# Kernel tuning notes

Measured on AMD Instinct MI355X. Metric: run time of the kernel, lower is better.

The kernel has to match this reference:

```python
import jax, jax.numpy as jnp
import numpy as np
from jax import lax

S, T, B = 32, 32, 512          # src len, tgt len, batch
H, E, A = 1024, 256, 1024      # hidden, embed, attention dim
VS, VT = 64, 70                # source / target char vocab
START = 1                      # data.tar_l2i[start_token]


def _gru_cell(gi, h, W_hh, b_hh):
    """torch GRUCell math. gi = x @ W_ih.T + b_ih, shape (B, 3H)."""
    gh = h @ W_hh.T + b_hh
    ir, iz, in_ = jnp.split(gi, 3, axis=-1)
    hr, hz, hn = jnp.split(gh, 3, axis=-1)
    r = jax.nn.sigmoid(ir + hr)
    z = jax.nn.sigmoid(iz + hz)
    n = jnp.tanh(in_ + r * hn)
    return (1.0 - z) * n + z * h


def setup_inputs() -> dict:
    key = jax.random.key(0)
    ks = jax.random.split(key, 16)
    n = lambda k, shp: jax.random.normal(k, shp, dtype=jnp.float32) * 0.05
    return {
        "source": jax.random.randint(ks[0], (S, B), 0, VS),
        "target": jax.random.randint(ks[1], (T, B), 0, VT),
        "teacher_forcing": 1,
        "emb_src": n(ks[2], (VS, E)),
        "W_ih_enc": n(ks[3], (3 * H, E)),
        "W_hh_enc": n(ks[4], (3 * H, H)),
        "b_ih_enc": n(ks[5], (3 * H,)),
        "b_hh_enc": n(ks[6], (3 * H,)),
        "emb_tgt": n(ks[7], (VT, E)),
        "W_attn": n(ks[8], (2 * H, A)),
        "b_attn": n(ks[9], (A,)),
        "v_attn": n(ks[10], (A,)),
        "W_ih_dec": n(ks[11], (3 * H, H + E)),
        "W_hh_dec": n(ks[12], (3 * H, H)),
        "b_ih_dec": n(ks[13], (3 * H,)),
        "b_hh_dec": n(ks[14], (3 * H,)),
        "W_out": n(ks[15], (H, VT)),
        "b_out": jnp.zeros((VT,), jnp.float32),
    }


def reference(source, target, teacher_forcing, emb_src, W_ih_enc, W_hh_enc,
              b_ih_enc, b_hh_enc, emb_tgt, W_attn, b_attn, v_attn,
              W_ih_dec, W_hh_dec, b_ih_dec, b_hh_dec, W_out, b_out):
    tf = bool(teacher_forcing)

    # ---------------- Encoder: GRU over (S, B) ----------------
    x_emb = emb_src[source]                                   # (S, B, E)
    # precompute input-to-hidden GEMM for all timesteps (big fused GEMM)
    gi_all = jnp.einsum('sbe,ge->sbg', x_emb, W_ih_enc) + b_ih_enc  # (S, B, 3H)

    def enc_step(h, gi_t):
        h = _gru_cell(gi_t, h, W_hh_enc, b_hh_enc)
        return h, h

    h0 = jnp.zeros((B, H), x_emb.dtype)
    h_enc, enc_ops = lax.scan(enc_step, h0, gi_all)           # enc_ops: (S, B, H)

    # ---------------- Decoder loop (t = 1 .. T-1) ----------------
    def dec_step(carry, tgt_t):
        h, x = carry
        emb = emb_tgt[x]                                      # (B, E)
        hx = jnp.broadcast_to(h[None], (S, B, H))
        feat = jnp.concatenate([hx, enc_ops], axis=-1)        # (S, B, 2H)
        energy = jnp.tanh(jnp.einsum('sbf,fa->sba', feat, W_attn) + b_attn)
        scores = energy @ v_attn                              # (S, B)
        alpha = jax.nn.softmax(scores, axis=0)                # over source positions
        ctx = jnp.einsum('sb,sbh->bh', alpha, enc_ops)        # (B, H)
        gi = jnp.concatenate([ctx, emb], axis=-1) @ W_ih_dec.T + b_ih_dec
        h_new = _gru_cell(gi, h, W_hh_dec, b_hh_dec)
        logits = h_new @ W_out + b_out                        # (B, VT)
        x_next = tgt_t if tf else jnp.argmax(logits, axis=1)
        return (h_new, x_next), (logits, alpha.T)             # attn row: (B, S)

    (_, _), (dec_logits, attn) = lax.scan(dec_step, (h_enc, target[0]), target[1:])

    # outputs[0] is the one-hot start token (outputs[:, :, start]=1, rows 1.. overwritten)
    row0 = jnp.zeros((B, VT), dec_logits.dtype).at[:, START].set(1.0)
    outputs = jnp.concatenate([row0[None], dec_logits], axis=0)  # (T, B, VT)
    return outputs, attn                                         # attn: (T-1, B, S)
```

## Files before the change

### kernel.cpp

```cpp
#include <hip/hip_runtime.h>
#include <hip/hip_bf16.h>

typedef __bf16 bfx8 __attribute__((ext_vector_type(8)));
typedef __bf16 bfx4 __attribute__((ext_vector_type(4)));
typedef float f32x4 __attribute__((ext_vector_type(4)));

#define MFMA __builtin_amdgcn_mfma_f32_16x16x32_bf16


__device__ __attribute__((aligned(256))) float  g_h[512 * 1024];
__device__ __attribute__((aligned(256))) float  g_hpart[512 * 1024];
__device__ __attribute__((aligned(256))) __bf16 g_hb[2][512 * 1024];
__device__ __attribute__((aligned(256))) __bf16 g_Adec[512 * 1280];
__device__ __attribute__((aligned(256))) __bf16 g_enc_ops[(size_t)32 * 512 * 1024];
__device__ __attribute__((aligned(256))) __bf16 g_enc_part[(size_t)32 * 512 * 1024];
__device__ __attribute__((aligned(256))) __bf16 g_sWhhe[(size_t)3072 * 1024];
__device__ __attribute__((aligned(256))) __bf16 g_sWihe[(size_t)3072 * 256];
__device__ __attribute__((aligned(256))) __bf16 g_sWhhd[(size_t)3072 * 1024];
__device__ __attribute__((aligned(256))) __bf16 g_sWihd[(size_t)3072 * 1280];
__device__ __attribute__((aligned(256))) __bf16 g_sWattnA[(size_t)1024 * 1024];
__device__ __attribute__((aligned(256))) __bf16 g_sWattnB[(size_t)1024 * 1024];
__device__ __attribute__((aligned(256))) __bf16 g_sWout[(size_t)128 * 1024];
__device__ __attribute__((aligned(256))) __bf16 g_embs[64 * 256];
__device__ __attribute__((aligned(256))) __bf16 g_embt[70 * 256];

__device__ __forceinline__ float fast_tanh(float x) {
    float cx = fminf(fmaxf(x, -15.f), 15.f);
    float e = __expf(-2.f * cx);
    return (1.f - e) / (1.f + e);
}

__global__ void k_cvt(const float* __restrict__ src, __bf16* __restrict__ dst,
                      int n4)
{
    int i = blockIdx.x * 256 + threadIdx.x;
    if (i >= n4) return;
    float4 v = ((const float4*)src)[i];
    __bf16 o[4] = {(__bf16)v.x, (__bf16)v.y, (__bf16)v.z, (__bf16)v.w};
    *(ushort2*)(dst + 4 * i) = *(ushort2*)o;
    *(ushort2*)(dst + 4 * i + 2) = *(ushort2*)(o + 2);
}

__global__ void swz_rm(const float* __restrict__ W, __bf16* __restrict__ out,
                       int nK, int total)
{
    int gid = blockIdx.x * 256 + threadIdx.x;
    if (gid >= total) return;
    int F = gid >> 6, L = gid & 63;
    int t = F / nK, c = F - t * nK;
    int K = nK * 32;
    const float* s = W + (size_t)(t * 16 + (L & 15)) * K + c * 32 + (L >> 4) * 8;
    __bf16 o[8];
#pragma unroll
    for (int u = 0; u < 8; u++) o[u] = (__bf16)s[u];
    *(uint4*)(out + (size_t)gid * 8) = *(uint4*)o;
}

__global__ void swz_cm(const float* __restrict__ W, __bf16* __restrict__ out,
                       int nK, int ldsrc, int nguard, int total)
{
    int gid = blockIdx.x * 256 + threadIdx.x;
    if (gid >= total) return;
    int F = gid >> 6, L = gid & 63;
    int t = F / nK, c = F - t * nK;
    int n = t * 16 + (L & 15);
    int k = c * 32 + (L >> 4) * 8;
    __bf16 o[8];
#pragma unroll
    for (int u = 0; u < 8; u++)
        o[u] = (n < nguard) ? (__bf16)W[(size_t)(k + u) * ldsrc + n] : (__bf16)0.f;
    *(uint4*)(out + (size_t)gid * 8) = *(uint4*)o;
}

__global__ void k_init(float* __restrict__ out)
{
    int idx = blockIdx.x * 256 + threadIdx.x;
    if (idx < 512 * 1024) { g_h[idx] = 0.f; g_hb[0][idx] = (__bf16)0.f; }
    if (idx < 512 * 70) out[idx] = (idx % 70 == 1) ? 1.f : 0.f;
}

__global__ __launch_bounds__(512, 1) void k_encpart(
    const __bf16* __restrict__ Amat, const __bf16* __restrict__ sW,
    __bf16* __restrict__ Cout)
{
    __shared__ __bf16 sA[64 * 1024];
    const int tid = threadIdx.x;
    const int w = tid >> 6, lane = tid & 63;
    const int r15 = lane & 15, q = lane >> 4;
    const int n0 = blockIdx.x * 256, m0 = blockIdx.y * 64;

#pragma unroll
    for (int i = 0; i < 16; i++) {
        int lin = tid + i * 512;
        int r = lin >> 7, U = lin & 127;
        uint4 v = *(const uint4*)(Amat + (size_t)(m0 + r) * 1024 + U * 8);
        *(uint4*)(sA + (r * 128 + (U ^ (r & 7))) * 8) = v;
    }
    __syncthreads();

    const int xk = r15 & 7;
    f32x4 acc[2][4];
#pragma unroll
    for (int nn = 0; nn < 2; nn++)
#pragma unroll
        for (int mf = 0; mf < 4; mf++) acc[nn][mf] = (f32x4){0.f, 0.f, 0.f, 0.f};

    const __bf16* wp0 = sW + ((size_t)(blockIdx.x * 16 + w * 2) * 32) * 512 + lane * 8;
    const __bf16* wp1 = wp0 + 32 * 512;
    const int ar0 = r15 * 1024;
    const int ar1 = (16 + r15) * 1024;
    const int ar2 = (32 + r15) * 1024;
    const int ar3 = (48 + r15) * 1024;

#pragma unroll 4
    for (int c = 0; c < 32; c++) {
        int us = ((c * 4 + q) ^ xk) * 8;
        bfx8 a0 = *(const bfx8*)(sA + ar0 + us);
        bfx8 a1 = *(const bfx8*)(sA + ar1 + us);
        bfx8 a2 = *(const bfx8*)(sA + ar2 + us);
        bfx8 a3 = *(const bfx8*)(sA + ar3 + us);
        bfx8 w0 = *(const bfx8*)(wp0 + c * 512);
        bfx8 w1 = *(const bfx8*)(wp1 + c * 512);
        acc[0][0] = MFMA(a0, w0, acc[0][0], 0, 0, 0);
        acc[0][1] = MFMA(a1, w0, acc[0][1], 0, 0, 0);
        acc[0][2] = MFMA(a2, w0, acc[0][2], 0, 0, 0);
        acc[0][3] = MFMA(a3, w0, acc[0][3], 0, 0, 0);
        acc[1][0] = MFMA(a0, w1, acc[1][0], 0, 0, 0);
        acc[1][1] = MFMA(a1, w1, acc[1][1], 0, 0, 0);
        acc[1][2] = MFMA(a2, w1, acc[1][2], 0, 0, 0);
        acc[1][3] = MFMA(a3, w1, acc[1][3], 0, 0, 0);
    }

#pragma unroll
    for (int nn = 0; nn < 2; nn++) {
        const int col = n0 + (w * 2 + nn) * 16 + r15;
#pragma unroll
        for (int mf = 0; mf < 4; mf++) {
#pragma unroll
            for (int reg = 0; reg < 4; reg++) {
                int row = m0 + mf * 16 + q * 4 + reg;
                Cout[(size_t)row * 1024 + col] = (__bf16)acc[nn][mf][reg];
            }
        }
    }
}

__global__ __launch_bounds__(512, 1) void gru_step(
    const __bf16* __restrict__ hb_in, __bf16* __restrict__ hb_out,
    const __bf16* __restrict__ sW1, const float* __restrict__ b1,
    const __bf16* __restrict__ sW2, const float* __restrict__ b2,
    int nK2, const int* __restrict__ src_t, int enc_t)
{
    __shared__ __bf16 sA1[32 * 1024];
    __shared__ __bf16 sA2[32 * 1280];
    const int tid = threadIdx.x;
    const int w = tid >> 6, lane = tid & 63;
    const int r15 = lane & 15, q = lane >> 4;
    const int j0 = blockIdx.x * 64, m0 = blockIdx.y * 32;
    const int jsub = w & 3;

#pragma unroll
    for (int i = 0; i < 8; i++) {
        int lin = tid + i * 512;
        int r = lin >> 7, U = lin & 127;
        uint4 v = *(const uint4*)(hb_in + (size_t)(m0 + r) * 1024 + U * 8);
        *(uint4*)(sA1 + (r * 128 + (U ^ (r & 7))) * 8) = v;
    }
    if (src_t) {
#pragma unroll
        for (int i = 0; i < 2; i++) {
            int lin = tid + i * 512;
            int r = lin >> 5, U = lin & 31;
            int sv = src_t[m0 + r];
            sv = (sv < 0) ? 0 : (sv > 63 ? 63 : sv);
            uint4 v = *(const uint4*)(g_embs + sv * 256 + U * 8);
            *(uint4*)(sA2 + (r * 32 + (U ^ (r & 7))) * 8) = v;
        }
    } else {
        for (int lin = tid; lin < 32 * 160; lin += 512) {
            int r = lin / 160, U = lin - r * 160;
            uint4 v = *(const uint4*)(g_Adec + (size_t)(m0 + r) * 1280 + U * 8);
            *(uint4*)(sA2 + (r * 160 + (U ^ (r & 7))) * 8) = v;
        }
    }
    __syncthreads();

    const size_t tb = (size_t)(blockIdx.x * 4 + jsub);
    const int xk = r15 & 7;
    f32x4 acc[3][2];
#pragma unroll
    for (int s = 0; s < 3; s++)
#pragma unroll
        for (int ms = 0; ms < 2; ms++) acc[s][ms] = (f32x4){0.f, 0.f, 0.f, 0.f};

    if (w < 4) {
        const __bf16* wp0 = sW1 + (tb * 32) * 512 + lane * 8;
        const __bf16* wp1 = sW1 + ((tb + 64) * 32) * 512 + lane * 8;
        const __bf16* wp2 = sW1 + ((tb + 128) * 32) * 512 + lane * 8;
        const int ar0 = r15 * 1024, ar1 = (16 + r15) * 1024;
#pragma unroll 4
        for (int c = 0; c < 32; c++) {
            int us = ((c * 4 + q) ^ xk) * 8;
            bfx8 a0 = *(const bfx8*)(sA1 + ar0 + us);
            bfx8 a1 = *(const bfx8*)(sA1 + ar1 + us);
            bfx8 w0 = *(const bfx8*)(wp0 + c * 512);
            bfx8 w1 = *(const bfx8*)(wp1 + c * 512);
            bfx8 w2 = *(const bfx8*)(wp2 + c * 512);
            acc[0][0] = MFMA(a0, w0, acc[0][0], 0, 0, 0);
            acc[0][1] = MFMA(a1, w0, acc[0][1], 0, 0, 0);
            acc[1][0] = MFMA(a0, w1, acc[1][0], 0, 0, 0);
            acc[1][1] = MFMA(a1, w1, acc[1][1], 0, 0, 0);
            acc[2][0] = MFMA(a0, w2, acc[2][0], 0, 0, 0);
            acc[2][1] = MFMA(a1, w2, acc[2][1], 0, 0, 0);
        }
    } else {
        const __bf16* wp0 = sW2 + (tb * (size_t)nK2) * 512 + lane * 8;
        const __bf16* wp1 = sW2 + ((tb + 64) * (size_t)nK2) * 512 + lane * 8;
        const __bf16* wp2 = sW2 + ((tb + 128) * (size_t)nK2) * 512 + lane * 8;
        const int ru = nK2 * 4;
        const int ar0 = r15 * ru * 8, ar1 = (16 + r15) * ru * 8;
#pragma unroll 4
        for (int c = 0; c < nK2; c++) {
            int us = ((c * 4 + q) ^ xk) * 8;
            bfx8 a0 = *(const bfx8*)(sA2 + ar0 + us);
            bfx8 a1 = *(const bfx8*)(sA2 + ar1 + us);
            bfx8 w0 = *(const bfx8*)(wp0 + c * 512);
            bfx8 w1 = *(const bfx8*)(wp1 + c * 512);
            bfx8 w2 = *(const bfx8*)(wp2 + c * 512);
            acc[0][0] = MFMA(a0, w0, acc[0][0], 0, 0, 0);
            acc[0][1] = MFMA(a1, w0, acc[0][1], 0, 0, 0);
            acc[1][0] = MFMA(a0, w1, acc[1][0], 0, 0, 0);
            acc[1][1] = MFMA(a1, w1, acc[1][1], 0, 0, 0);
            acc[2][0] = MFMA(a0, w2, acc[2][0], 0, 0, 0);
            acc[2][1] = MFMA(a1, w2, acc[2][1], 0, 0, 0);
        }
    }
    __syncthreads();
    float* sGi = (float*)sA2;
    if (w >= 4) {
#pragma unroll
        for (int s = 0; s < 3; s++)
#pragma unroll
            for (int ms = 0; ms < 2; ms++)
#pragma unroll
                for (int reg = 0; reg < 4; reg++)
                    sGi[((s * 4 + jsub) * 32 + ms * 16 + q * 4 + reg) * 16 + r15] =
                        acc[s][ms][reg];
    }
    __syncthreads();
    if (w < 4) {
        const int jj = j0 + jsub * 16 + r15;
        const float bb1[3] = {b1[jj], b1[1024 + jj], b1[2048 + jj]};
        const float bb2[3] = {b2[jj], b2[1024 + jj], b2[2048 + jj]};
#pragma unroll
        for (int ms = 0; ms < 2; ms++) {
#pragma unroll
            for (int reg = 0; reg < 4; reg++) {
                int bl = ms * 16 + q * 4 + reg;
                int b_ = m0 + bl;
                float gh0 = acc[0][ms][reg] + bb1[0];
                float gh1 = acc[1][ms][reg] + bb1[1];
                float gh2 = acc[2][ms][reg] + bb1[2];
                float gi0 = sGi[((0 * 4 + jsub) * 32 + bl) * 16 + r15] + bb2[0];
                float gi1 = sGi[((1 * 4 + jsub) * 32 + bl) * 16 + r15] + bb2[1];
                float gi2 = sGi[((2 * 4 + jsub) * 32 + bl) * 16 + r15] + bb2[2];
                float r = 1.f / (1.f + __expf(-(gi0 + gh0)));
                float z = 1.f / (1.f + __expf(-(gi1 + gh1)));
                float n = fast_tanh(gi2 + r * gh2);
                size_t off = (size_t)b_ * 1024 + jj;
                float hv = (1.f - z) * n + z * g_h[off];
                g_h[off] = hv;
                hb_out[off] = (__bf16)hv;
                if (enc_t >= 0)
                    g_enc_ops[(size_t)enc_t * 524288 + off] = (__bf16)hv;
            }
        }
    }
}

__global__ __launch_bounds__(256) void k_hl(
    const __bf16* __restrict__ src, const float* __restrict__ battn,
    const float* __restrict__ bout, int lrow, float* __restrict__ outp)
{
    __shared__ __bf16 sA[32 * 1024];
    const int tid = threadIdx.x;
    const int w = tid >> 6, lane = tid & 63;
    const int r15 = lane & 15, q = lane >> 4;
    const int bx = blockIdx.x, m0 = blockIdx.y * 32;

#pragma unroll
    for (int i = 0; i < 16; i++) {
        int lin = tid + i * 256;
        int r = lin >> 7, U = lin & 127;
        uint4 v = *(const uint4*)(src + (size_t)(m0 + r) * 1024 + U * 8);
        *(uint4*)(sA + (r * 128 + (U ^ (r & 7))) * 8) = v;
    }
    __syncthreads();

    const __bf16* sW;
    int n;
    if (bx < 16) {
        sW = g_sWattnA;
        n = bx * 64 + w * 16 + r15;
    } else {
        if (lrow < 0) return;
        sW = g_sWout;
        n = (bx - 16) * 64 + w * 16 + r15;
    }
    const size_t tb = (size_t)((bx < 16 ? bx : bx - 16) * 4 + w);
    const __bf16* wp = sW + (tb * 32) * 512 + lane * 8;
    const int xk = r15 & 7;
    const int ar0 = r15 * 1024, ar1 = (16 + r15) * 1024;

    f32x4 acc[2];
    acc[0] = (f32x4){0.f, 0.f, 0.f, 0.f};
    acc[1] = (f32x4){0.f, 0.f, 0.f, 0.f};
#pragma unroll 4
    for (int c = 0; c < 32; c++) {
        int us = ((c * 4 + q) ^ xk) * 8;
        bfx8 a0 = *(const bfx8*)(sA + ar0 + us);
        bfx8 a1 = *(const bfx8*)(sA + ar1 + us);
        bfx8 wv = *(const bfx8*)(wp + c * 512);
        acc[0] = MFMA(a0, wv, acc[0], 0, 0, 0);
        acc[1] = MFMA(a1, wv, acc[1], 0, 0, 0);
    }

    if (bx < 16) {
        float bv = battn[n];
#pragma unroll
        for (int ms = 0; ms < 2; ms++)
#pragma unroll
            for (int reg = 0; reg < 4; reg++)
                g_hpart[(size_t)(m0 + ms * 16 + q * 4 + reg) * 1024 + n] =
                    acc[ms][reg] + bv;
    } else if (n < 70) {
        float bv = bout[n];
#pragma unroll
        for (int ms = 0; ms < 2; ms++)
#pragma unroll
            for (int reg = 0; reg < 4; reg++)
                outp[(size_t)lrow * 35840 +
                     (size_t)(m0 + ms * 16 + q * 4 + reg) * 70 + n] =
                    acc[ms][reg] + bv;
    }
}

__global__ __launch_bounds__(256) void k_attn(
    int j, const int* __restrict__ target, const int* __restrict__ tf,
    const float* __restrict__ v_attn, float* __restrict__ out)
{
    const int b = blockIdx.x, tid = threadIdx.x;
    const int lane = tid & 63, wave = tid >> 6;
    __shared__ float sc[32], sal[32];
    __shared__ int sx;
    if (wave == 0) {
        int xv;
        if (j == 0) xv = target[b];
        else if (*tf) xv = target[j * 512 + b];
        else {
            const float* row = out + (size_t)j * 35840 + b * 70;
            float bv = row[lane]; int bi = lane;
            if (lane < 6) {
                float v2 = row[lane + 64];
                if (v2 > bv) { bv = v2; bi = lane + 64; }
            }
#pragma unroll
            for (int off = 32; off; off >>= 1) {
                float ov = __shfl_down(bv, off);
                int   oi = __shfl_down(bi, off);
                if (ov > bv || (ov == bv && oi < bi)) { bv = ov; bi = oi; }
            }
            xv = bi;
        }
        if (lane == 0) sx = (xv < 0) ? 0 : (xv > 69 ? 69 : xv);
    }
    float hpv[16], vsv[16];
    {
        const float* hp = g_hpart + (size_t)b * 1024;
#pragma unroll
        for (int u = 0; u < 8; u++) {
            hpv[u]     = hp[lane * 8 + u];
            hpv[8 + u] = hp[512 + lane * 8 + u];
            vsv[u]     = v_attn[lane * 8 + u];
            vsv[8 + u] = v_attn[512 + lane * 8 + u];
        }
    }
    __syncthreads();
    g_Adec[(size_t)b * 1280 + 1024 + tid] = g_embt[sx * 256 + tid];
    for (int s = wave * 8; s < wave * 8 + 8; s++) {
        const __bf16* ep = g_enc_part + ((size_t)s * 512 + b) * 1024;
        bfx8 e0 = *(const bfx8*)(ep + lane * 8);
        bfx8 e1 = *(const bfx8*)(ep + 512 + lane * 8);
        float part = 0.f;
#pragma unroll
        for (int u = 0; u < 8; u++) {
            part += vsv[u]     * fast_tanh((float)e0[u] + hpv[u]);
            part += vsv[8 + u] * fast_tanh((float)e1[u] + hpv[8 + u]);
        }
#pragma unroll
        for (int off = 32; off; off >>= 1) part += __shfl_down(part, off);
        if (lane == 0) sc[s] = part;
    }
    __syncthreads();
    float mx = sc[0];
#pragma unroll
    for (int s = 1; s < 32; s++) mx = fmaxf(mx, sc[s]);
    float den = 0.f;
#pragma unroll
    for (int s = 0; s < 32; s++) den += __expf(sc[s] - mx);
    float rden = 1.f / den;
    if (tid < 32) {
        float al = __expf(sc[tid] - mx) * rden;
        sal[tid] = al;
        out[1146880 + (size_t)j * 16384 + b * 32 + tid] = al;
    }
    __syncthreads();
    float c0 = 0, c1 = 0, c2 = 0, c3 = 0;
    const __bf16* eo = g_enc_ops + (size_t)b * 1024 + tid * 4;
#pragma unroll 4
    for (int s = 0; s < 32; s++) {
        bfx4 e = *(const bfx4*)(eo + (size_t)s * 524288);
        float al = sal[s];
        c0 += al * (float)e[0]; c1 += al * (float)e[1];
        c2 += al * (float)e[2]; c3 += al * (float)e[3];
    }
    bfx4 o = {(__bf16)c0, (__bf16)c1, (__bf16)c2, (__bf16)c3};
    *(bfx4*)(&g_Adec[(size_t)b * 1280 + tid * 4]) = o;
}

extern "C" void kernel_launch(void* const* d_in, const int* in_sizes, int n_in,
                              void* d_out, int out_size, void* d_ws, size_t ws_size,
                              hipStream_t stream)
{
    const int*   source   = (const int*)d_in[0];
    const int*   target   = (const int*)d_in[1];
    const int*   tf       = (const int*)d_in[2];
    const float* emb_src  = (const float*)d_in[3];
    const float* W_ih_enc = (const float*)d_in[4];
    const float* W_hh_enc = (const float*)d_in[5];
    const float* b_ih_enc = (const float*)d_in[6];
    const float* b_hh_enc = (const float*)d_in[7];
    const float* emb_tgt  = (const float*)d_in[8];
    const float* W_attn   = (const float*)d_in[9];
    const float* b_attn   = (const float*)d_in[10];
    const float* v_attn   = (const float*)d_in[11];
    const float* W_ih_dec = (const float*)d_in[12];
    const float* W_hh_dec = (const float*)d_in[13];
    const float* b_ih_dec = (const float*)d_in[14];
    const float* b_hh_dec = (const float*)d_in[15];
    const float* W_out    = (const float*)d_in[16];
    const float* b_out    = (const float*)d_in[17];
    float* out = (float*)d_out;

    void *p_hb, *p_sWhhe, *p_sWihe, *p_sWhhd, *p_sWihd, *p_sWattnA, *p_sWattnB,
         *p_sWout, *p_embs, *p_embt, *p_enc_ops, *p_enc_part;
    hipGetSymbolAddress(&p_hb,       HIP_SYMBOL(g_hb));
    hipGetSymbolAddress(&p_sWhhe,    HIP_SYMBOL(g_sWhhe));
    hipGetSymbolAddress(&p_sWihe,    HIP_SYMBOL(g_sWihe));
    hipGetSymbolAddress(&p_sWhhd,    HIP_SYMBOL(g_sWhhd));
    hipGetSymbolAddress(&p_sWihd,    HIP_SYMBOL(g_sWihd));
    hipGetSymbolAddress(&p_sWattnA,  HIP_SYMBOL(g_sWattnA));
    hipGetSymbolAddress(&p_sWattnB,  HIP_SYMBOL(g_sWattnB));
    hipGetSymbolAddress(&p_sWout,    HIP_SYMBOL(g_sWout));
    hipGetSymbolAddress(&p_embs,     HIP_SYMBOL(g_embs));
    hipGetSymbolAddress(&p_embt,     HIP_SYMBOL(g_embt));
    hipGetSymbolAddress(&p_enc_ops,  HIP_SYMBOL(g_enc_ops));
    hipGetSymbolAddress(&p_enc_part, HIP_SYMBOL(g_enc_part));
    __bf16* hb0 = (__bf16*)p_hb;
    __bf16* hb1 = hb0 + 512 * 1024;

    k_cvt<<<16, 256, 0, stream>>>(emb_src, (__bf16*)p_embs, 64 * 256 / 4);
    k_cvt<<<18, 256, 0, stream>>>(emb_tgt, (__bf16*)p_embt, 70 * 256 / 4);
    swz_rm<<<1536, 256, 0, stream>>>(W_hh_enc, (__bf16*)p_sWhhe, 32, 393216);
    swz_rm<<<384,  256, 0, stream>>>(W_ih_enc, (__bf16*)p_sWihe, 8,  98304);
    swz_rm<<<1536, 256, 0, stream>>>(W_hh_dec, (__bf16*)p_sWhhd, 32, 393216);
    swz_rm<<<1920, 256, 0, stream>>>(W_ih_dec, (__bf16*)p_sWihd, 40, 491520);
    swz_cm<<<512,  256, 0, stream>>>(W_attn, (__bf16*)p_sWattnA, 32, 1024, 1024, 131072);
    swz_cm<<<512,  256, 0, stream>>>(W_attn + (size_t)1024 * 1024,
                                     (__bf16*)p_sWattnB, 32, 1024, 1024, 131072);
    swz_cm<<<64,   256, 0, stream>>>(W_out,  (__bf16*)p_sWout,   32, 70,   70,   16384);
    k_init<<<2048, 256, 0, stream>>>(out);

    for (int t = 0; t < 32; t++) {
        __bf16* hin  = (t & 1) ? hb1 : hb0;
        __bf16* hout = (t & 1) ? hb0 : hb1;
        gru_step<<<dim3(16, 16), 512, 0, stream>>>(
            hin, hout, (__bf16*)p_sWhhe, b_hh_enc,
            (__bf16*)p_sWihe, b_ih_enc, 8, source + t * 512, t);
    }

    k_encpart<<<dim3(4, 256), 512, 0, stream>>>(
        (__bf16*)p_enc_ops, (__bf16*)p_sWattnB, (__bf16*)p_enc_part);

    k_hl<<<dim3(18, 16), 256, 0, stream>>>(hb0, b_attn, b_out, -1, out);

    for (int j = 0; j < 31; j++) {
        __bf16* hin  = (j & 1) ? hb1 : hb0;
        __bf16* hout = (j & 1) ? hb0 : hb1;
        k_attn<<<512, 256, 0, stream>>>(j, target, tf, v_attn, out);
        gru_step<<<dim3(16, 16), 512, 0, stream>>>(
            hin, hout, (__bf16*)p_sWhhd, b_hh_dec,
            (__bf16*)p_sWihd, b_ih_dec, 40, nullptr, -1);
        k_hl<<<dim3(18, 16), 256, 0, stream>>>(hout, b_attn, b_out, j + 1, out);
    }
}
```

Measured before the change: 2.551 ms.

## Double-buffer encoder input GEMM and rebalance GRU step K-loop across warps

Result: no change. 2.550 ms (-0.1%).

```diff
diff --git a/kernel.cpp b/kernel.cpp
--- a/kernel.cpp
+++ b/kernel.cpp
@@ -79,23 +79,32 @@
     if (idx < 512 * 70) out[idx] = (idx % 70 == 1) ? 1.f : 0.f;
 }
 
-__global__ __launch_bounds__(512, 1) void k_encpart(
+__global__ __launch_bounds__(512, 4) void k_encpart(
     const __bf16* __restrict__ Amat, const __bf16* __restrict__ sW,
     __bf16* __restrict__ Cout)
 {
-    __shared__ __bf16 sA[64 * 1024];
+    __shared__ __bf16 sA[2][64 * 256];
     const int tid = threadIdx.x;
     const int w = tid >> 6, lane = tid & 63;
     const int r15 = lane & 15, q = lane >> 4;
     const int n0 = blockIdx.x * 256, m0 = blockIdx.y * 64;
 
-#pragma unroll
-    for (int i = 0; i < 16; i++) {
+    int sr[4], sv[4], so[4];
+#pragma unroll
+    for (int i = 0; i < 4; i++) {
         int lin = tid + i * 512;
-        int r = lin >> 7, U = lin & 127;
-        uint4 v = *(const uint4*)(Amat + (size_t)(m0 + r) * 1024 + U * 8);
-        *(uint4*)(sA + (r * 128 + (U ^ (r & 7))) * 8) = v;
-    }
+        sr[i] = lin >> 5;
+        sv[i] = lin & 31;
+        so[i] = (sr[i] * 32 + (sv[i] ^ (sr[i] & 7))) * 8;
+    }
+
+    uint4 regs[4];
+#pragma unroll
+    for (int i = 0; i < 4; i++)
+        regs[i] = *(const uint4*)(Amat + (size_t)(m0 + sr[i]) * 1024 + sv[i] * 8);
+#pragma unroll
+    for (int i = 0; i < 4; i++)
+        *(uint4*)(&sA[0][so[i]]) = regs[i];
     __syncthreads();
 
     const int xk = r15 & 7;
@@ -107,28 +116,45 @@
 
     const __bf16* wp0 = sW + ((size_t)(blockIdx.x * 16 + w * 2) * 32) * 512 + lane * 8;
     const __bf16* wp1 = wp0 + 32 * 512;
-    const int ar0 = r15 * 1024;
-    const int ar1 = (16 + r15) * 1024;
-    const int ar2 = (32 + r15) * 1024;
-    const int ar3 = (48 + r15) * 1024;
-
-#pragma unroll 4
-    for (int c = 0; c < 32; c++) {
-        int us = ((c * 4 + q) ^ xk) * 8;
-        bfx8 a0 = *(const bfx8*)(sA + ar0 + us);
-        bfx8 a1 = *(const bfx8*)(sA + ar1 + us);
-        bfx8 a2 = *(const bfx8*)(sA + ar2 + us);
-        bfx8 a3 = *(const bfx8*)(sA + ar3 + us);
-        bfx8 w0 = *(const bfx8*)(wp0 + c * 512);
-        bfx8 w1 = *(const bfx8*)(wp1 + c * 512);
-        acc[0][0] = MFMA(a0, w0, acc[0][0], 0, 0, 0);
-        acc[0][1] = MFMA(a1, w0, acc[0][1], 0, 0, 0);
-        acc[0][2] = MFMA(a2, w0, acc[0][2], 0, 0, 0);
-        acc[0][3] = MFMA(a3, w0, acc[0][3], 0, 0, 0);
-        acc[1][0] = MFMA(a0, w1, acc[1][0], 0, 0, 0);
-        acc[1][1] = MFMA(a1, w1, acc[1][1], 0, 0, 0);
-        acc[1][2] = MFMA(a2, w1, acc[1][2], 0, 0, 0);
-        acc[1][3] = MFMA(a3, w1, acc[1][3], 0, 0, 0);
+    const int ar0 = r15 * 256;
+    const int ar1 = (16 + r15) * 256;
+    const int ar2 = (32 + r15) * 256;
+    const int ar3 = (48 + r15) * 256;
+
+    for (int kc = 0; kc < 4; kc++) {
+        if (kc < 3) {
+#pragma unroll
+            for (int i = 0; i < 4; i++)
+                regs[i] = *(const uint4*)(Amat + (size_t)(m0 + sr[i]) * 1024 +
+                                          (kc + 1) * 256 + sv[i] * 8);
+        }
+        const __bf16* sAb = sA[kc & 1];
+        const __bf16* wq0 = wp0 + kc * 8 * 512;
+        const __bf16* wq1 = wp1 + kc * 8 * 512;
+#pragma unroll
+        for (int c = 0; c < 8; c++) {
+            int us = ((c * 4 + q) ^ xk) * 8;
+            bfx8 a0 = *(const bfx8*)(sAb + ar0 + us);
+            bfx8 a1 = *(const bfx8*)(sAb + ar1 + us);
+            bfx8 a2 = *(const bfx8*)(sAb + ar2 + us);
+            bfx8 a3 = *(const bfx8*)(sAb + ar3 + us);
+            bfx8 w0 = *(const bfx8*)(wq0 + c * 512);
+            bfx8 w1 = *(const bfx8*)(wq1 + c * 512);
+            acc[0][0] = MFMA(a0, w0, acc[0][0], 0, 0, 0);
+            acc[0][1] = MFMA(a1, w0, acc[0][1], 0, 0, 0);
+            acc[0][2] = MFMA(a2, w0, acc[0][2], 0, 0, 0);
+            acc[0][3] = MFMA(a3, w0, acc[0][3], 0, 0, 0);
+            acc[1][0] = MFMA(a0, w1, acc[1][0], 0, 0, 0);
+            acc[1][1] = MFMA(a1, w1, acc[1][1], 0, 0, 0);
+            acc[1][2] = MFMA(a2, w1, acc[1][2], 0, 0, 0);
+            acc[1][3] = MFMA(a3, w1, acc[1][3], 0, 0, 0);
+        }
+        if (kc < 3) {
+#pragma unroll
+            for (int i = 0; i < 4; i++)
+                *(uint4*)(&sA[(kc + 1) & 1][so[i]]) = regs[i];
+            __syncthreads();
+        }
     }
 
 #pragma unroll
@@ -144,6 +170,22 @@
         }
     }
 }
+
+#define GH_BODY(ACC)                                              \
+    {                                                             \
+        int us = ((c * 4 + q) ^ xk) * 8;                          \
+        bfx8 a0 = *(const bfx8*)(sA1 + br0 + us);                 \
+        bfx8 a1 = *(const bfx8*)(sA1 + br1 + us);                 \
+        bfx8 w0 = *(const bfx8*)(xp0 + c * 512);                  \
+        bfx8 w1 = *(const bfx8*)(xp1 + c * 512);                  \
+        bfx8 w2 = *(const bfx8*)(xp2 + c * 512);                  \
+        ACC[0][0] = MFMA(a0, w0, ACC[0][0], 0, 0, 0);             \
+        ACC[0][1] = MFMA(a1, w0, ACC[0][1], 0, 0, 0);             \
+        ACC[1][0] = MFMA(a0, w1, ACC[1][0], 0, 0, 0);             \
+        ACC[1][1] = MFMA(a1, w1, ACC[1][1], 0, 0, 0);             \
+        ACC[2][0] = MFMA(a0, w2, ACC[2][0], 0, 0, 0);             \
+        ACC[2][1] = MFMA(a1, w2, ACC[2][1], 0, 0, 0);             \
+    }
 
 __global__ __launch_bounds__(512, 1) void gru_step(
     const __bf16* __restrict__ hb_in, __bf16* __restrict__ hb_out,
@@ -194,15 +236,28 @@
         for (int ms = 0; ms < 2; ms++) acc[s][ms] = (f32x4){0.f, 0.f, 0.f, 0.f};
 
     if (w < 4) {
-        const __bf16* wp0 = sW1 + (tb * 32) * 512 + lane * 8;
-        const __bf16* wp1 = sW1 + ((tb + 64) * 32) * 512 + lane * 8;
-        const __bf16* wp2 = sW1 + ((tb + 128) * 32) * 512 + lane * 8;
-        const int ar0 = r15 * 1024, ar1 = (16 + r15) * 1024;
+        const __bf16* xp0 = sW1 + (tb * 32) * 512 + lane * 8;
+        const __bf16* xp1 = sW1 + ((tb + 64) * 32) * 512 + lane * 8;
+        const __bf16* xp2 = sW1 + ((tb + 128) * 32) * 512 + lane * 8;
+        const int br0 = r15 * 1024, br1 = (16 + r15) * 1024;
+        if (src_t) {
 #pragma unroll 4
-        for (int c = 0; c < 32; c++) {
+            for (int c = 0; c < 20; c++) GH_BODY(acc)
+        } else {
+#pragma unroll 8
+            for (int c = 0; c < 32; c++) GH_BODY(acc)
+        }
+    } else {
+        const __bf16* wp0 = sW2 + (tb * (size_t)nK2) * 512 + lane * 8;
+        const __bf16* wp1 = sW2 + ((tb + 64) * (size_t)nK2) * 512 + lane * 8;
+        const __bf16* wp2 = sW2 + ((tb + 128) * (size_t)nK2) * 512 + lane * 8;
+        const int ru = nK2 * 4;
+        const int gr0 = r15 * ru * 8, gr1 = (16 + r15) * ru * 8;
+#pragma unroll 8
+        for (int c = 0; c < nK2; c++) {
             int us = ((c * 4 + q) ^ xk) * 8;
-            bfx8 a0 = *(const bfx8*)(sA1 + ar0 + us);
-            bfx8 a1 = *(const bfx8*)(sA1 + ar1 + us);
+            bfx8 a0 = *(const bfx8*)(sA2 + gr0 + us);
+            bfx8 a1 = *(const bfx8*)(sA2 + gr1 + us);
             bfx8 w0 = *(const bfx8*)(wp0 + c * 512);
             bfx8 w1 = *(const bfx8*)(wp1 + c * 512);
             bfx8 w2 = *(const bfx8*)(wp2 + c * 512);
@@ -213,26 +268,27 @@
             acc[2][0] = MFMA(a0, w2, acc[2][0], 0, 0, 0);
             acc[2][1] = MFMA(a1, w2, acc[2][1], 0, 0, 0);
         }
-    } else {
-        const __bf16* wp0 = sW2 + (tb * (size_t)nK2) * 512 + lane * 8;
-        const __bf16* wp1 = sW2 + ((tb + 64) * (size_t)nK2) * 512 + lane * 8;
-        const __bf16* wp2 = sW2 + ((tb + 128) * (size_t)nK2) * 512 + lane * 8;
-        const int ru = nK2 * 4;
-        const int ar0 = r15 * ru * 8, ar1 = (16 + r15) * ru * 8;
+        if (src_t) {
+            f32x4 acc2[3][2];
+#pragma unroll
+            for (int s = 0; s < 3; s++)
+#pragma unroll
+                for (int ms = 0; ms < 2; ms++) acc2[s][ms] = (f32x4){0.f, 0.f, 0.f, 0.f};
+            const __bf16* xp0 = sW1 + (tb * 32) * 512 + lane * 8;
+            const __bf16* xp1 = sW1 + ((tb + 64) * 32) * 512 + lane * 8;
+            const __bf16* xp2 = sW1 + ((tb + 128) * 32) * 512 + lane * 8;
+            const int br0 = r15 * 1024, br1 = (16 + r15) * 1024;
 #pragma unroll 4
-        for (int c = 0; c < nK2; c++) {
-            int us = ((c * 4 + q) ^ xk) * 8;
-            bfx8 a0 = *(const bfx8*)(sA2 + ar0 + us);
-            bfx8 a1 = *(const bfx8*)(sA2 + ar1 + us);
-            bfx8 w0 = *(const bfx8*)(wp0 + c * 512);
-            bfx8 w1 = *(const bfx8*)(wp1 + c * 512);
-            bfx8 w2 = *(const bfx8*)(wp2 + c * 512);
-            acc[0][0] = MFMA(a0, w0, acc[0][0], 0, 0, 0);
-            acc[0][1] = MFMA(a1, w0, acc[0][1], 0, 0, 0);
-            acc[1][0] = MFMA(a0, w1, acc[1][0], 0, 0, 0);
-            acc[1][1] = MFMA(a1, w1, acc[1][1], 0, 0, 0);
-            acc[2][0] = MFMA(a0, w2, acc[2][0], 0, 0, 0);
-            acc[2][1] = MFMA(a1, w2, acc[2][1], 0, 0, 0);
+            for (int c = 20; c < 32; c++) GH_BODY(acc2)
+            float* sGh = (float*)sA2 + 6144;
+#pragma unroll
+            for (int s = 0; s < 3; s++)
+#pragma unroll
+                for (int ms = 0; ms < 2; ms++)
+#pragma unroll
+                    for (int reg = 0; reg < 4; reg++)
+                        sGh[((s * 4 + jsub) * 32 + ms * 16 + q * 4 + reg) * 16 + r15] =
+                            acc2[s][ms][reg];
         }
     }
     __syncthreads();
@@ -252,15 +308,22 @@
         const int jj = j0 + jsub * 16 + r15;
         const float bb1[3] = {b1[jj], b1[1024 + jj], b1[2048 + jj]};
         const float bb2[3] = {b2[jj], b2[1024 + jj], b2[2048 + jj]};
+        const float* sGh = (const float*)sA2 + 6144;
 #pragma unroll
         for (int ms = 0; ms < 2; ms++) {
 #pragma unroll
             for (int reg = 0; reg < 4; reg++) {
                 int bl = ms * 16 + q * 4 + reg;
                 int b_ = m0 + bl;
-                float gh0 = acc[0][ms][reg] + bb1[0];
-                float gh1 = acc[1][ms][reg] + bb1[1];
-                float gh2 = acc[2][ms][reg] + bb1[2];
+                float e0 = 0.f, e1 = 0.f, e2 = 0.f;
+                if (src_t) {
+                    e0 = sGh[((0 * 4 + jsub) * 32 + bl) * 16 + r15];
+                    e1 = sGh[((1 * 4 + jsub) * 32 + bl) * 16 + r15];
+                    e2 = sGh[((2 * 4 + jsub) * 32 + bl) * 16 + r15];
+                }
+                float gh0 = acc[0][ms][reg] + bb1[0] + e0;
+                float gh1 = acc[1][ms][reg] + bb1[1] + e1;
+                float gh2 = acc[2][ms][reg] + bb1[2] + e2;
                 float gi0 = sGi[((0 * 4 + jsub) * 32 + bl) * 16 + r15] + bb2[0];
                 float gi1 = sGi[((1 * 4 + jsub) * 32 + bl) * 16 + r15] + bb2[1];
                 float gi2 = sGi[((2 * 4 + jsub) * 32 + bl) * 16 + r15] + bb2[2];
@@ -315,7 +378,7 @@
     f32x4 acc[2];
     acc[0] = (f32x4){0.f, 0.f, 0.f, 0.f};
     acc[1] = (f32x4){0.f, 0.f, 0.f, 0.f};
-#pragma unroll 4
+#pragma unroll 8
     for (int c = 0; c < 32; c++) {
         int us = ((c * 4 + q) ^ xk) * 8;
         bfx8 a0 = *(const bfx8*)(sA + ar0 + us);
```
